# Optimization experiments

Hardware: AMD Instinct MI355X
Metric: run time of the kernel (lower is better)

## Reference

```python
import jax, jax.numpy as jnp
import numpy as np

DIM = 1024
SEGMENT_SIZE = 1024
DILATION_RATE = 2

def setup_inputs() -> dict:
    key = jax.random.key(0)
    x = jax.random.normal(key, (4, 8192, DIM), dtype=jnp.float32)
    return {"x": x}

def reference(x) -> jnp.ndarray:
    B, S, D = x.shape
    pad = (-S) % SEGMENT_SIZE
    x = jnp.pad(x, ((0, 0), (0, pad), (0, 0)))
    # [B, n_seg, segment_size, D]
    x = x.reshape(B, -1, SEGMENT_SIZE, D)
    # dilation: strided slice within each segment -> [B, n_seg, seg', D]
    x = x[:, :, ::DILATION_RATE, :]
    q = k = v = x
    scale = 1.0 / jnp.sqrt(jnp.asarray(D, dtype=x.dtype))
    # attention within each segment over dilated tokens (non-causal, no dropout)
    scores = jnp.einsum('bsqd,bskd->bsqk', q, k) * scale
    probs = jax.nn.softmax(scores, axis=-1)
    attn = jnp.einsum('bsqk,bskd->bsqd', probs, v)
    # flatten segments back to a (shortened, dilated) sequence
    return attn.reshape(B, -1, D)
```

## Files before the change

### kernel.cpp

```cpp
#include <hip/hip_runtime.h>


typedef float          f32x4  __attribute__((ext_vector_type(4)));
typedef short          bf16x8 __attribute__((ext_vector_type(8)));

#define MFMA16(a, b, c) __builtin_amdgcn_mfma_f32_16x16x32_bf16((a), (b), (c), 0, 0, 0)

static __device__ __forceinline__ unsigned short f2bf(float f) {
    unsigned u = __float_as_uint(f);
    u = (u + 0x7fffu + ((u >> 16) & 1u)) >> 16;
    return (unsigned short)u;
}

static __device__ __forceinline__ void async_cp16(const unsigned short* g, unsigned short* l) {
    __builtin_amdgcn_global_load_lds((const __attribute__((address_space(1))) unsigned int*)g,
                                     (__attribute__((address_space(3))) unsigned int*)l,
                                     16, 0, 0);
}

static __device__ __forceinline__ void stage_tile(const unsigned short* __restrict__ src,
                                                  unsigned short* lds,
                                                  int row_stride, int col0,
                                                  int wave, int lane) {
    const int pr = lane >> 3;
    const int lc = (lane & 7) ^ pr;
    #pragma unroll
    for (int c = 0; c < 4; ++c) {
        const int chunk = wave * 4 + c;
        async_cp16(src + (size_t)(chunk * 8 + pr) * row_stride + col0 + lc * 8,
                   lds + chunk * 512);
    }
}

__global__ __launch_bounds__(256) void k_prep(const float* __restrict__ x,
                                              unsigned short* __restrict__ Xb,
                                              unsigned short* __restrict__ VT) {
    const int kb = blockIdx.x, db = blockIdx.y, g = blockIdx.z;
    const int t = threadIdx.x;
    __shared__ unsigned short Ts[64][72];
    {
        const int r = t >> 2, q = t & 3;
        const float* src = x + ((size_t)g << 20) + (size_t)(kb * 64 + r) * 2048 + db * 64 + q * 16;
        alignas(16) unsigned short tmp[16];
        #pragma unroll
        for (int i = 0; i < 4; ++i) {
            const float4 v = *reinterpret_cast<const float4*>(src + i * 4);
            tmp[i * 4 + 0] = f2bf(v.x); tmp[i * 4 + 1] = f2bf(v.y);
            tmp[i * 4 + 2] = f2bf(v.z); tmp[i * 4 + 3] = f2bf(v.w);
        }
        unsigned short* xb = Xb + ((size_t)g * 512 + kb * 64 + r) * 1024 + db * 64 + q * 16;
        *reinterpret_cast<uint4*>(xb)     = *reinterpret_cast<const uint4*>(&tmp[0]);
        *reinterpret_cast<uint4*>(xb + 8) = *reinterpret_cast<const uint4*>(&tmp[8]);
        *reinterpret_cast<uint4*>(&Ts[r][q * 16])     = *reinterpret_cast<const uint4*>(&tmp[0]);
        *reinterpret_cast<uint4*>(&Ts[r][q * 16 + 8]) = *reinterpret_cast<const uint4*>(&tmp[8]);
    }
    __syncthreads();
    {
        const int dl = t >> 2, kq = t & 3;
        alignas(16) unsigned short o[16];
        #pragma unroll
        for (int j = 0; j < 16; ++j) o[j] = Ts[kq * 16 + j][dl];
        unsigned short* vt = VT + ((size_t)g * 1024 + db * 64 + dl) * 512 + kb * 64 + kq * 16;
        *reinterpret_cast<uint4*>(vt)     = *reinterpret_cast<const uint4*>(&o[0]);
        *reinterpret_cast<uint4*>(vt + 8) = *reinterpret_cast<const uint4*>(&o[8]);
    }
}

__global__ __launch_bounds__(256) void k_scores(const unsigned short* __restrict__ Xb,
                                                unsigned short* __restrict__ T,
                                                float* __restrict__ Lsum) {
    const int g = blockIdx.x, nb = blockIdx.y, mb = blockIdx.z;
    const int tid = threadIdx.x, wave = tid >> 6, lane = tid & 63;
    const int g4 = lane >> 4, n16 = lane & 15;
    const int wr = wave & 1, wc = wave >> 1;

    __shared__ unsigned short As[128 * 64];
    __shared__ unsigned short Bs[128 * 64];
    __shared__ float red[4][64];

    const unsigned short* Ag = Xb + ((size_t)g * 512 + mb * 128) * 1024;
    const unsigned short* Bg = Xb + ((size_t)g * 512 + nb * 128) * 1024;

    f32x4 acc[16];
    const f32x4 vzero = {0.f, 0.f, 0.f, 0.f};
    #pragma unroll
    for (int i = 0; i < 16; ++i) acc[i] = vzero;

    for (int kt = 0; kt < 16; ++kt) {
        if (kt) __syncthreads();
        stage_tile(Ag, As, 1024, kt * 64, wave, lane);
        stage_tile(Bg, Bs, 1024, kt * 64, wave, lane);
        __syncthreads();
        #pragma unroll
        for (int ks = 0; ks < 2; ++ks) {
            const int sw = ((ks * 4 + g4) ^ (n16 & 7)) * 8;
            bf16x8 a[4], b[4];
            #pragma unroll
            for (int i = 0; i < 4; ++i)
                a[i] = *reinterpret_cast<const bf16x8*>(&As[(wr * 64 + i * 16 + n16) * 64 + sw]);
            #pragma unroll
            for (int j = 0; j < 4; ++j)
                b[j] = *reinterpret_cast<const bf16x8*>(&Bs[(wc * 64 + j * 16 + n16) * 64 + sw]);
            #pragma unroll
            for (int i = 0; i < 4; ++i)
                #pragma unroll
                for (int j = 0; j < 4; ++j)
                    acc[i * 4 + j] = MFMA16(a[i], b[j], acc[i * 4 + j]);
        }
    }

    float rs[4][4];
    #pragma unroll
    for (int i = 0; i < 4; ++i)
        #pragma unroll
        for (int r = 0; r < 4; ++r) rs[i][r] = 0.f;

    unsigned short* Tg = T + ((size_t)g * 512 + mb * 128 + wr * 64) * 512 + nb * 128 + wc * 64;
    #pragma unroll
    for (int i = 0; i < 4; ++i)
        #pragma unroll
        for (int j = 0; j < 4; ++j)
            #pragma unroll
            for (int r = 0; r < 4; ++r) {
                const float e = __expf(acc[i * 4 + j][r] * 0.03125f);
                rs[i][r] += e;
                Tg[(size_t)(i * 16 + g4 * 4 + r) * 512 + j * 16 + n16] = f2bf(e);
            }

    #pragma unroll
    for (int d = 1; d < 16; d <<= 1)
        #pragma unroll
        for (int i = 0; i < 4; ++i)
            #pragma unroll
            for (int r = 0; r < 4; ++r)
                rs[i][r] += __shfl_xor(rs[i][r], d, 64);
    if (n16 == 0) {
        #pragma unroll
        for (int i = 0; i < 4; ++i)
            #pragma unroll
            for (int r = 0; r < 4; ++r)
                red[wave][i * 16 + g4 * 4 + r] = rs[i][r];
    }
    __syncthreads();
    if (tid < 128) {
        const int h = tid >> 6, idx = tid & 63;
        atomicAdd(&Lsum[g * 512 + mb * 128 + h * 64 + idx],
                  red[h][idx] + red[h + 2][idx]);
    }
}

__global__ __launch_bounds__(256) void k_pv(const unsigned short* __restrict__ T,
                                            const unsigned short* __restrict__ VT,
                                            const float* __restrict__ Lsum,
                                            float* __restrict__ out) {
    const int g = blockIdx.x, nb = blockIdx.y, mb = blockIdx.z;
    const int tid = threadIdx.x, wave = tid >> 6, lane = tid & 63;
    const int g4 = lane >> 4, n16 = lane & 15;
    const int wr = wave & 1, wc = wave >> 1;

    __shared__ unsigned short As[128 * 64];
    __shared__ unsigned short Bs[128 * 64];
    __shared__ float Linv[128];

    if (tid < 128) Linv[tid] = 1.0f / Lsum[g * 512 + mb * 128 + tid];

    const unsigned short* Ag = T  + ((size_t)g * 512  + mb * 128) * 512;
    const unsigned short* Bg = VT + ((size_t)g * 1024 + nb * 128) * 512;

    f32x4 acc[16];
    const f32x4 vzero = {0.f, 0.f, 0.f, 0.f};
    #pragma unroll
    for (int i = 0; i < 16; ++i) acc[i] = vzero;

    for (int kt = 0; kt < 8; ++kt) {
        __syncthreads();
        stage_tile(Ag, As, 512, kt * 64, wave, lane);
        stage_tile(Bg, Bs, 512, kt * 64, wave, lane);
        __syncthreads();
        #pragma unroll
        for (int ks = 0; ks < 2; ++ks) {
            const int sw = ((ks * 4 + g4) ^ (n16 & 7)) * 8;
            bf16x8 a[4], b[4];
            #pragma unroll
            for (int i = 0; i < 4; ++i)
                a[i] = *reinterpret_cast<const bf16x8*>(&As[(wr * 64 + i * 16 + n16) * 64 + sw]);
            #pragma unroll
            for (int j = 0; j < 4; ++j)
                b[j] = *reinterpret_cast<const bf16x8*>(&Bs[(wc * 64 + j * 16 + n16) * 64 + sw]);
            #pragma unroll
            for (int i = 0; i < 4; ++i)
                #pragma unroll
                for (int j = 0; j < 4; ++j)
                    acc[i * 4 + j] = MFMA16(a[i], b[j], acc[i * 4 + j]);
        }
    }

    float li[4][4];
    #pragma unroll
    for (int i = 0; i < 4; ++i)
        #pragma unroll
        for (int r = 0; r < 4; ++r)
            li[i][r] = Linv[wr * 64 + i * 16 + g4 * 4 + r];

    float* og = out + ((size_t)g * 512 + mb * 128 + wr * 64) * 1024 + nb * 128 + wc * 64;
    #pragma unroll
    for (int i = 0; i < 4; ++i)
        #pragma unroll
        for (int j = 0; j < 4; ++j)
            #pragma unroll
            for (int r = 0; r < 4; ++r)
                og[(size_t)(i * 16 + g4 * 4 + r) * 1024 + j * 16 + n16] =
                    acc[i * 4 + j][r] * li[i][r];
}

extern "C" void kernel_launch(void* const* d_in, const int* in_sizes, int n_in,
                              void* d_out, int out_size, void* d_ws, size_t ws_size,
                              hipStream_t stream) {
    const float* x = (const float*)d_in[0];
    float* out = (float*)d_out;

    unsigned short* T  = (unsigned short*)d_ws;
    unsigned short* Xb = T  + (size_t)32 * 512 * 512;
    unsigned short* VT = Xb + (size_t)32 * 512 * 1024;
    float*          Ls = (float*)(VT + (size_t)32 * 1024 * 512);

    hipMemsetAsync(Ls, 0, 32 * 512 * sizeof(float), stream);
    k_prep  <<<dim3(8, 16, 32), 256, 0, stream>>>(x, Xb, VT);
    k_scores<<<dim3(32, 4, 4),  256, 0, stream>>>(Xb, T, Ls);
    k_pv    <<<dim3(32, 8, 4),  256, 0, stream>>>(T, VT, Ls, out);
}
```

Baseline: 249.3 us.

## Fuse score and PV kernels into one attention kernel with LDS-resident probabilities

Merges the scores and PV GEMM kernels into a single k_attn kernel. Each block handles 32 query rows and keeps the full 32x512 unnormalized exp probabilities in LDS, which removes the global T buffer, the atomic row-sum accumulation and the memset. Each block now re-streams all K and V for its group. Tiles shrink to 32 rows per block, which lowers MFMA reuse per loaded K/V tile and raises global/L2 traffic in exchange for fewer launches and no round-trip of the probability matrix.

New measurement: 258.1 us. 3.5% more time.

```diff
diff --git a/kernel.cpp b/kernel.cpp
--- a/kernel.cpp
+++ b/kernel.cpp
@@ -16,20 +16,6 @@
     __builtin_amdgcn_global_load_lds((const __attribute__((address_space(1))) unsigned int*)g,
                                      (__attribute__((address_space(3))) unsigned int*)l,
                                      16, 0, 0);
-}
-
-static __device__ __forceinline__ void stage_tile(const unsigned short* __restrict__ src,
-                                                  unsigned short* lds,
-                                                  int row_stride, int col0,
-                                                  int wave, int lane) {
-    const int pr = lane >> 3;
-    const int lc = (lane & 7) ^ pr;
-    #pragma unroll
-    for (int c = 0; c < 4; ++c) {
-        const int chunk = wave * 4 + c;
-        async_cp16(src + (size_t)(chunk * 8 + pr) * row_stride + col0 + lc * 8,
-                   lds + chunk * 512);
-    }
 }
 
 __global__ __launch_bounds__(256) void k_prep(const float* __restrict__ x,
@@ -66,151 +52,129 @@
     }
 }
 
-__global__ __launch_bounds__(256) void k_scores(const unsigned short* __restrict__ Xb,
-                                                unsigned short* __restrict__ T,
-                                                float* __restrict__ Lsum) {
-    const int g = blockIdx.x, nb = blockIdx.y, mb = blockIdx.z;
+__global__ __launch_bounds__(512, 4) void k_attn(const unsigned short* __restrict__ Xb,
+                                                 const unsigned short* __restrict__ VT,
+                                                 float* __restrict__ out) {
+    const int g = blockIdx.x, mb = blockIdx.y;
     const int tid = threadIdx.x, wave = tid >> 6, lane = tid & 63;
     const int g4 = lane >> 4, n16 = lane & 15;
     const int wr = wave & 1, wc = wave >> 1;
+    const int pr = lane >> 3;
+    const int plc = (lane & 7) ^ pr;
 
-    __shared__ unsigned short As[128 * 64];
-    __shared__ unsigned short Bs[128 * 64];
-    __shared__ float red[4][64];
+    __shared__ unsigned short Ps[32 * 512];
+    __shared__ unsigned short Qs[32 * 64];
+    __shared__ unsigned short Ks[256 * 64];
+    __shared__ float red[8][16];
+    __shared__ float Linv[32];
 
-    const unsigned short* Ag = Xb + ((size_t)g * 512 + mb * 128) * 1024;
-    const unsigned short* Bg = Xb + ((size_t)g * 512 + nb * 128) * 1024;
+    const unsigned short* Qg = Xb + ((size_t)g * 512 + mb * 32) * 1024;
+    const unsigned short* Kg = Xb + (size_t)g * 512 * 1024;
+    const unsigned short* Vg = VT + (size_t)g * 1024 * 512;
 
-    f32x4 acc[16];
+    float rs[4] = {0.f, 0.f, 0.f, 0.f};
     const f32x4 vzero = {0.f, 0.f, 0.f, 0.f};
-    #pragma unroll
-    for (int i = 0; i < 16; ++i) acc[i] = vzero;
 
-    for (int kt = 0; kt < 16; ++kt) {
-        if (kt) __syncthreads();
-        stage_tile(Ag, As, 1024, kt * 64, wave, lane);
-        stage_tile(Bg, Bs, 1024, kt * 64, wave, lane);
-        __syncthreads();
+    for (int nb2 = 0; nb2 < 2; ++nb2) {
+        f32x4 acc[4];
         #pragma unroll
-        for (int ks = 0; ks < 2; ++ks) {
-            const int sw = ((ks * 4 + g4) ^ (n16 & 7)) * 8;
-            bf16x8 a[4], b[4];
+        for (int j = 0; j < 4; ++j) acc[j] = vzero;
+
+        for (int kt = 0; kt < 16; ++kt) {
+            __syncthreads();
+            if (wave < 4)
+                async_cp16(Qg + (size_t)(wave * 8 + pr) * 1024 + kt * 64 + plc * 8,
+                           Qs + wave * 512);
             #pragma unroll
-            for (int i = 0; i < 4; ++i)
-                a[i] = *reinterpret_cast<const bf16x8*>(&As[(wr * 64 + i * 16 + n16) * 64 + sw]);
+            for (int c = 0; c < 4; ++c) {
+                const int row = wave * 32 + c * 8 + pr;
+                async_cp16(Kg + (size_t)(nb2 * 256 + row) * 1024 + kt * 64 + plc * 8,
+                           Ks + (wave * 4 + c) * 512);
+            }
+            __syncthreads();
             #pragma unroll
-            for (int j = 0; j < 4; ++j)
-                b[j] = *reinterpret_cast<const bf16x8*>(&Bs[(wc * 64 + j * 16 + n16) * 64 + sw]);
-            #pragma unroll
-            for (int i = 0; i < 4; ++i)
+            for (int ks = 0; ks < 2; ++ks) {
+                const int sw = ((ks * 4 + g4) ^ (n16 & 7)) * 8;
+                const bf16x8 a = *reinterpret_cast<const bf16x8*>(&Qs[(wr * 16 + n16) * 64 + sw]);
+                bf16x8 b[4];
                 #pragma unroll
                 for (int j = 0; j < 4; ++j)
-                    acc[i * 4 + j] = MFMA16(a[i], b[j], acc[i * 4 + j]);
+                    b[j] = *reinterpret_cast<const bf16x8*>(&Ks[(wc * 64 + j * 16 + n16) * 64 + sw]);
+                #pragma unroll
+                for (int j = 0; j < 4; ++j) acc[j] = MFMA16(a, b[j], acc[j]);
+            }
         }
-    }
 
-    float rs[4][4];
-    #pragma unroll
-    for (int i = 0; i < 4; ++i)
-        #pragma unroll
-        for (int r = 0; r < 4; ++r) rs[i][r] = 0.f;
-
-    unsigned short* Tg = T + ((size_t)g * 512 + mb * 128 + wr * 64) * 512 + nb * 128 + wc * 64;
-    #pragma unroll
-    for (int i = 0; i < 4; ++i)
         #pragma unroll
         for (int j = 0; j < 4; ++j)
             #pragma unroll
             for (int r = 0; r < 4; ++r) {
-                const float e = __expf(acc[i * 4 + j][r] * 0.03125f);
-                rs[i][r] += e;
-                Tg[(size_t)(i * 16 + g4 * 4 + r) * 512 + j * 16 + n16] = f2bf(e);
+                const float e = __expf(acc[j][r] * 0.03125f);
+                rs[r] += e;
+                const int row = wr * 16 + g4 * 4 + r;
+                const int c = nb2 * 256 + wc * 64 + j * 16 + n16;
+                const int lc = c >> 3;
+                Ps[row * 512 + (((lc ^ (row & 7)) << 3) | (c & 7))] = f2bf(e);
             }
+    }
 
     #pragma unroll
     for (int d = 1; d < 16; d <<= 1)
         #pragma unroll
-        for (int i = 0; i < 4; ++i)
-            #pragma unroll
-            for (int r = 0; r < 4; ++r)
-                rs[i][r] += __shfl_xor(rs[i][r], d, 64);
+        for (int r = 0; r < 4; ++r) rs[r] += __shfl_xor(rs[r], d, 64);
     if (n16 == 0) {
         #pragma unroll
-        for (int i = 0; i < 4; ++i)
-            #pragma unroll
-            for (int r = 0; r < 4; ++r)
-                red[wave][i * 16 + g4 * 4 + r] = rs[i][r];
+        for (int r = 0; r < 4; ++r) red[wave][g4 * 4 + r] = rs[r];
     }
     __syncthreads();
-    if (tid < 128) {
-        const int h = tid >> 6, idx = tid & 63;
-        atomicAdd(&Lsum[g * 512 + mb * 128 + h * 64 + idx],
-                  red[h][idx] + red[h + 2][idx]);
+    if (tid < 32) {
+        const int w2 = tid >> 4, r16 = tid & 15;
+        Linv[tid] = 1.0f / (red[w2][r16] + red[2 + w2][r16] + red[4 + w2][r16] + red[6 + w2][r16]);
     }
-}
+    __syncthreads();
 
-__global__ __launch_bounds__(256) void k_pv(const unsigned short* __restrict__ T,
-                                            const unsigned short* __restrict__ VT,
-                                            const float* __restrict__ Lsum,
-                                            float* __restrict__ out) {
-    const int g = blockIdx.x, nb = blockIdx.y, mb = blockIdx.z;
-    const int tid = threadIdx.x, wave = tid >> 6, lane = tid & 63;
-    const int g4 = lane >> 4, n16 = lane & 15;
-    const int wr = wave & 1, wc = wave >> 1;
+    float li[4];
+    #pragma unroll
+    for (int r = 0; r < 4; ++r) li[r] = Linv[wr * 16 + g4 * 4 + r];
 
-    __shared__ unsigned short As[128 * 64];
-    __shared__ unsigned short Bs[128 * 64];
-    __shared__ float Linv[128];
+    float* og = out + ((size_t)g * 512 + mb * 32) * 1024;
+    const int mrow = wr * 16 + n16;
+    for (int db2 = 0; db2 < 4; ++db2) {
+        f32x4 acc[4];
+        #pragma unroll
+        for (int j = 0; j < 4; ++j) acc[j] = vzero;
 
-    if (tid < 128) Linv[tid] = 1.0f / Lsum[g * 512 + mb * 128 + tid];
-
-    const unsigned short* Ag = T  + ((size_t)g * 512  + mb * 128) * 512;
-    const unsigned short* Bg = VT + ((size_t)g * 1024 + nb * 128) * 512;
-
-    f32x4 acc[16];
-    const f32x4 vzero = {0.f, 0.f, 0.f, 0.f};
-    #pragma unroll
-    for (int i = 0; i < 16; ++i) acc[i] = vzero;
-
-    for (int kt = 0; kt < 8; ++kt) {
-        __syncthreads();
-        stage_tile(Ag, As, 512, kt * 64, wave, lane);
-        stage_tile(Bg, Bs, 512, kt * 64, wave, lane);
-        __syncthreads();
-        #pragma unroll
-        for (int ks = 0; ks < 2; ++ks) {
-            const int sw = ((ks * 4 + g4) ^ (n16 & 7)) * 8;
-            bf16x8 a[4], b[4];
+        for (int kt2 = 0; kt2 < 8; ++kt2) {
+            __syncthreads();
             #pragma unroll
-            for (int i = 0; i < 4; ++i)
-                a[i] = *reinterpret_cast<const bf16x8*>(&As[(wr * 64 + i * 16 + n16) * 64 + sw]);
+            for (int c = 0; c < 4; ++c) {
+                const int row = wave * 32 + c * 8 + pr;
+                async_cp16(Vg + (size_t)(db2 * 256 + row) * 512 + kt2 * 64 + plc * 8,
+                           Ks + (wave * 4 + c) * 512);
+            }
+            __syncthreads();
             #pragma unroll
-            for (int j = 0; j < 4; ++j)
-                b[j] = *reinterpret_cast<const bf16x8*>(&Bs[(wc * 64 + j * 16 + n16) * 64 + sw]);
-            #pragma unroll
-            for (int i = 0; i < 4; ++i)
+            for (int ks = 0; ks < 2; ++ks) {
+                const int lc = kt2 * 8 + ks * 4 + g4;
+                const bf16x8 a = *reinterpret_cast<const bf16x8*>(
+                    &Ps[mrow * 512 + ((lc ^ (mrow & 7)) << 3)]);
+                const int sw = ((ks * 4 + g4) ^ (n16 & 7)) * 8;
+                bf16x8 b[4];
                 #pragma unroll
                 for (int j = 0; j < 4; ++j)
-                    acc[i * 4 + j] = MFMA16(a[i], b[j], acc[i * 4 + j]);
+                    b[j] = *reinterpret_cast<const bf16x8*>(&Ks[(wc * 64 + j * 16 + n16) * 64 + sw]);
+                #pragma unroll
+                for (int j = 0; j < 4; ++j) acc[j] = MFMA16(a, b[j], acc[j]);
+            }
         }
-    }
 
-    float li[4][4];
-    #pragma unroll
-    for (int i = 0; i < 4; ++i)
-        #pragma unroll
-        for (int r = 0; r < 4; ++r)
-            li[i][r] = Linv[wr * 64 + i * 16 + g4 * 4 + r];
-
-    float* og = out + ((size_t)g * 512 + mb * 128 + wr * 64) * 1024 + nb * 128 + wc * 64;
-    #pragma unroll
-    for (int i = 0; i < 4; ++i)
         #pragma unroll
         for (int j = 0; j < 4; ++j)
             #pragma unroll
             for (int r = 0; r < 4; ++r)
-                og[(size_t)(i * 16 + g4 * 4 + r) * 1024 + j * 16 + n16] =
-                    acc[i * 4 + j][r] * li[i][r];
+                og[(size_t)(wr * 16 + g4 * 4 + r) * 1024 + db2 * 256 + wc * 64 + j * 16 + n16]
+                    = acc[j][r] * li[r];
+    }
 }
 
 extern "C" void kernel_launch(void* const* d_in, const int* in_sizes, int n_in,
@@ -219,13 +183,9 @@
     const float* x = (const float*)d_in[0];
     float* out = (float*)d_out;
 
-    unsigned short* T  = (unsigned short*)d_ws;
-    unsigned short* Xb = T  + (size_t)32 * 512 * 512;
+    unsigned short* Xb = (unsigned short*)d_ws;
     unsigned short* VT = Xb + (size_t)32 * 512 * 1024;
-    float*          Ls = (float*)(VT + (size_t)32 * 1024 * 512);
 
-    hipMemsetAsync(Ls, 0, 32 * 512 * sizeof(float), stream);
-    k_prep  <<<dim3(8, 16, 32), 256, 0, stream>>>(x, Xb, VT);
-    k_scores<<<dim3(32, 4, 4),  256, 0, stream>>>(Xb, T, Ls);
-    k_pv    <<<dim3(32, 8, 4),  256, 0, stream>>>(T, VT, Ls, out);
+    k_prep<<<dim3(8, 16, 32), 256, 0, stream>>>(x, Xb, VT);
+    k_attn<<<dim3(32, 16),    512, 0, stream>>>(Xb, VT, out);
 }
```

## Exploit score symmetry: compute upper-triangle tiles and mirror-write transposes

Applied to the files above, without the earlier changes.

Because q=k, the score matrix X·Xᵀ is symmetric. k_scores now computes only the 10 upper-triangular 128x128 tiles per group instead of 16, writes each exp tile plus its transpose, and accumulates column sums into the row-sum buffer for the mirrored half. The memset of the row-sum buffer is folded into k_prep to remove a separate launch. The trade is fewer blocks, which lowers parallelism, and uncoalesced 8-byte transposed stores.

After: 246.7 us. No clear change (-1.1%).

```diff
diff --git a/kernel.cpp b/kernel.cpp
--- a/kernel.cpp
+++ b/kernel.cpp
@@ -34,9 +34,14 @@
 
 __global__ __launch_bounds__(256) void k_prep(const float* __restrict__ x,
                                               unsigned short* __restrict__ Xb,
-                                              unsigned short* __restrict__ VT) {
+                                              unsigned short* __restrict__ VT,
+                                              float* __restrict__ Lsum) {
     const int kb = blockIdx.x, db = blockIdx.y, g = blockIdx.z;
     const int t = threadIdx.x;
+    if (kb == 0 && db == 0) {
+        Lsum[g * 512 + t] = 0.f;
+        Lsum[g * 512 + 256 + t] = 0.f;
+    }
     __shared__ unsigned short Ts[64][72];
     {
         const int r = t >> 2, q = t & 3;
@@ -69,7 +74,12 @@
 __global__ __launch_bounds__(256) void k_scores(const unsigned short* __restrict__ Xb,
                                                 unsigned short* __restrict__ T,
                                                 float* __restrict__ Lsum) {
-    const int g = blockIdx.x, nb = blockIdx.y, mb = blockIdx.z;
+    const int g = blockIdx.x, item = blockIdx.y;
+    const int mb = (item < 4) ? 0 : (item < 7) ? 1 : (item < 9) ? 2 : 3;
+    const int start = (mb == 0) ? 0 : (mb == 1) ? 4 : (mb == 2) ? 7 : 9;
+    const int nb = mb + (item - start);
+    const bool diag = (mb == nb);
+
     const int tid = threadIdx.x, wave = tid >> 6, lane = tid & 63;
     const int g4 = lane >> 4, n16 = lane & 15;
     const int wr = wave & 1, wc = wave >> 1;
@@ -110,22 +120,37 @@
     }
 
     float rs[4][4];
+    float cs[4];
     #pragma unroll
     for (int i = 0; i < 4; ++i)
         #pragma unroll
         for (int r = 0; r < 4; ++r) rs[i][r] = 0.f;
+    #pragma unroll
+    for (int j = 0; j < 4; ++j) cs[j] = 0.f;
 
     unsigned short* Tg = T + ((size_t)g * 512 + mb * 128 + wr * 64) * 512 + nb * 128 + wc * 64;
-    #pragma unroll
-    for (int i = 0; i < 4; ++i)
-        #pragma unroll
-        for (int j = 0; j < 4; ++j)
+    unsigned short* Tm = T + ((size_t)g * 512 + nb * 128 + wc * 64) * 512 + mb * 128 + wr * 64;
+    #pragma unroll
+    for (int i = 0; i < 4; ++i)
+        #pragma unroll
+        for (int j = 0; j < 4; ++j) {
+            unsigned pk[2];
             #pragma unroll
             for (int r = 0; r < 4; ++r) {
                 const float e = __expf(acc[i * 4 + j][r] * 0.03125f);
                 rs[i][r] += e;
-                Tg[(size_t)(i * 16 + g4 * 4 + r) * 512 + j * 16 + n16] = f2bf(e);
+                cs[j] += e;
+                const unsigned short h = f2bf(e);
+                Tg[(size_t)(i * 16 + g4 * 4 + r) * 512 + j * 16 + n16] = h;
+                if (r & 1) pk[r >> 1] |= (unsigned)h << 16;
+                else       pk[r >> 1]  = h;
             }
+            if (!diag) {
+                *reinterpret_cast<uint2*>(
+                    &Tm[(size_t)(j * 16 + n16) * 512 + i * 16 + g4 * 4]) =
+                    make_uint2(pk[0], pk[1]);
+            }
+        }
 
     #pragma unroll
     for (int d = 1; d < 16; d <<= 1)
@@ -141,6 +166,18 @@
             for (int r = 0; r < 4; ++r)
                 red[wave][i * 16 + g4 * 4 + r] = rs[i][r];
     }
+
+    if (!diag) {
+        #pragma unroll
+        for (int j = 0; j < 4; ++j) {
+            float c = cs[j];
+            c += __shfl_xor(c, 16, 64);
+            c += __shfl_xor(c, 32, 64);
+            if (g4 == 0)
+                atomicAdd(&Lsum[g * 512 + nb * 128 + wc * 64 + j * 16 + n16], c);
+        }
+    }
+
     __syncthreads();
     if (tid < 128) {
         const int h = tid >> 6, idx = tid & 63;
@@ -224,8 +261,7 @@
     unsigned short* VT = Xb + (size_t)32 * 512 * 1024;
     float*          Ls = (float*)(VT + (size_t)32 * 1024 * 512);
 
-    hipMemsetAsync(Ls, 0, 32 * 512 * sizeof(float), stream);
-    k_prep  <<<dim3(8, 16, 32), 256, 0, stream>>>(x, Xb, VT);
-    k_scores<<<dim3(32, 4, 4),  256, 0, stream>>>(Xb, T, Ls);
+    k_prep  <<<dim3(8, 16, 32), 256, 0, stream>>>(x, Xb, VT, Ls);
+    k_scores<<<dim3(32, 10),    256, 0, stream>>>(Xb, T, Ls);
     k_pv    <<<dim3(32, 8, 4),  256, 0, stream>>>(T, VT, Ls, out);
 }
```
